# Kernel tuning notes

Hardware: AMD Instinct MI355X
Metric: run time of the kernel (lower is better)

## Reference

```python
import jax, jax.numpy as jnp
import numpy as np

N_NODES = 100000
N_EDGES = 1600000
NUM_RELS = 8
IN_FEAT = 128
OUT_FEAT = 128


def setup_inputs() -> dict:
    key = jax.random.key(0)
    k1, k2, k3, k4, k5 = jax.random.split(key, 5)
    feat = jax.random.normal(k1, (N_NODES, IN_FEAT), dtype=jnp.float32)
    weight = jax.random.normal(k2, (NUM_RELS, IN_FEAT, OUT_FEAT), dtype=jnp.float32) * 0.05
    src = jax.random.randint(k3, (N_EDGES,), 0, N_NODES, dtype=jnp.int64 if jax.config.jax_enable_x64 else jnp.int32)
    dst = jax.random.randint(k4, (N_EDGES,), 0, N_NODES, dtype=jnp.int64 if jax.config.jax_enable_x64 else jnp.int32)
    etypes = jax.random.randint(k5, (N_EDGES,), 0, NUM_RELS, dtype=jnp.int64 if jax.config.jax_enable_x64 else jnp.int32)
    return {"feat": feat, "weight": weight, "src": src, "dst": dst, "etypes": etypes}


def reference(feat, weight, src, dst, etypes):
    # RGCN segment_mm: per edge e, message m_e = feat[src[e]] @ weight[etypes[e]],
    # then sum-aggregate messages into destination nodes.
    # The torch module sorts edges by etype only so segment_mm can run a grouped
    # GEMM; the scatter-sum aggregation is order-independent, so sorting does not
    # change the math. We compute all per-relation projections densely (small R)
    # and gather the right one per edge -- equivalent math, fully vectorized.
    proj = jnp.einsum('ni,rio->rno', feat, weight)      # [R, N, out]
    m = proj[etypes, src]                               # [E, out] gather per edge
    out = jax.ops.segment_sum(m, dst, num_segments=feat.shape[0])  # [N, out]
    return out
```

## Files before the change

kernel.cpp:

```cpp
#include <hip/hip_runtime.h>
#include <hip/hip_bf16.h>


#define FEAT 128
#define LDG 136
#define LDSS 136
#define CAP 512
#define CHUNK 128

typedef __attribute__((ext_vector_type(8))) short short8;
typedef __attribute__((ext_vector_type(8))) __bf16 bf16x8;
typedef __attribute__((ext_vector_type(4))) float f32x4;

__device__ __forceinline__ unsigned f2bf(float x) {
    union { float f; unsigned u; } v; v.f = x;
    unsigned r = v.u + 0x7FFFu + ((v.u >> 16) & 1u);
    return r >> 16;
}

__global__ void cvt_feat_kernel(const float* __restrict__ f,
                                ushort* __restrict__ o, int n8) {
    int i = blockIdx.x * blockDim.x + threadIdx.x;
    if (i >= n8) return;
    const float4* f4 = (const float4*)f;
    float4 a = f4[2 * i], b = f4[2 * i + 1];
    union { ushort u[8]; int4 v; } pk;
    pk.u[0] = f2bf(a.x); pk.u[1] = f2bf(a.y); pk.u[2] = f2bf(a.z); pk.u[3] = f2bf(a.w);
    pk.u[4] = f2bf(b.x); pk.u[5] = f2bf(b.y); pk.u[6] = f2bf(b.z); pk.u[7] = f2bf(b.w);
    ((int4*)o)[i] = pk.v;
}

__global__ void cvt_w_kernel(const float* __restrict__ w,
                             ushort* __restrict__ wt, int total, int KW) {
    int i = blockIdx.x * blockDim.x + threadIdx.x;
    if (i >= total) return;
    int n = i / KW;
    int rk = i - n * KW;
    int r = rk >> 7, k = rk & 127;
    wt[i] = (ushort)f2bf(w[(r << 14) + (k << 7) + n]);
}

__global__ void scatter_kernel(const int* __restrict__ dst,
                               const int* __restrict__ et,
                               const int* __restrict__ src, int E, int R,
                               int sbits, int* __restrict__ cursor,
                               int* __restrict__ recs) {
    int i = blockIdx.x * blockDim.x + threadIdx.x;
    int stride = gridDim.x * blockDim.x;
    for (; i < E; i += stride) {
        int d = dst[i];
        int b = (d >> 7) * R + et[i];
        int p = atomicAdd(&cursor[b], 1);
        if (p < CAP) recs[(size_t)b * CAP + p] = src[i] | ((d & 127) << sbits);
    }
}

__global__ __launch_bounds__(256, 2)
void fused_kernel(const ushort* __restrict__ featb,
                  const ushort* __restrict__ wtb,
                  const int* __restrict__ recs,
                  const int* __restrict__ cursor,
                  float* __restrict__ out, int N, int R, int KW, int sbits) {
    __shared__ __align__(16) ushort GS[CHUNK * LDG];
    __shared__ __align__(16) ushort dlv[CHUNK];

    int t = threadIdx.x;
    int qid = t >> 4, c = t & 15;
    int lane = t & 63, wid = t >> 6;
    int lm = lane & 15, lq = lane >> 4;
    int blk = blockIdx.x, base = blk * 128;
    int mq = (wid >> 1) * 64, nq = (wid & 1) * 64;
    int smask = (1 << sbits) - 1;

    f32x4 acc[16];
    #pragma unroll
    for (int i = 0; i < 16; i++) acc[i] = (f32x4){0.f, 0.f, 0.f, 0.f};

    for (int r = 0; r < R; r++) {
        int bkt = blk * R + r;
        int ecnt = cursor[bkt];
        if (ecnt <= 0) continue;
        if (ecnt > CAP) ecnt = CAP;
        const int* rb = recs + (size_t)bkt * CAP;

        f32x4 accS[16];
        #pragma unroll
        for (int i = 0; i < 16; i++) accS[i] = (f32x4){0.f, 0.f, 0.f, 0.f};

        for (int c0 = 0; c0 < ecnt; c0 += CHUNK) {
            int rcv[8]; uint4 gvv[8];
            #pragma unroll
            for (int p = 0; p < 8; p++) {
                int j = c0 + p * 16 + qid;
                rcv[p] = (j < ecnt) ? rb[j] : -1;
            }
            #pragma unroll
            for (int p = 0; p < 8; p++) {
                if (rcv[p] >= 0)
                    gvv[p] = *(const uint4*)(featb +
                             (size_t)(rcv[p] & smask) * FEAT + c * 8);
                else
                    gvv[p] = (uint4){0u, 0u, 0u, 0u};
            }
            #pragma unroll
            for (int p = 0; p < 8; p++)
                *(uint4*)&GS[(p * 16 + qid) * LDG + c * 8] = gvv[p];
            if (c == 0) {
                #pragma unroll
                for (int p = 0; p < 8; p++)
                    dlv[p * 16 + qid] = (rcv[p] >= 0)
                        ? (ushort)((rcv[p] >> sbits) & 127) : (ushort)0xFFFF;
            }
            __syncthreads();

            #pragma unroll
            for (int ks = 0; ks < 4; ks++) {
                int kof = ks * 32 + lq * 8;
                union { ushort u[8]; uint4 v; } dlw;
                dlw.v = *(const uint4*)&dlv[kof];
                short8 paf[4];
                #pragma unroll
                for (int tm = 0; tm < 4; tm++) {
                    ushort row = (ushort)(mq + tm * 16 + lm);
                    union { ushort u[8]; short8 s; } pa;
                    #pragma unroll
                    for (int q = 0; q < 8; q++)
                        pa.u[q] = (dlw.u[q] == row) ? (ushort)0x3F80 : (ushort)0;
                    paf[tm] = pa.s;
                }
                short8 bgf[4];
                #pragma unroll
                for (int tn = 0; tn < 4; tn++) {
                    int col = nq + tn * 16 + lm;
                    union { ushort u[8]; short8 s; } bb;
                    #pragma unroll
                    for (int q = 0; q < 8; q++)
                        bb.u[q] = GS[(kof + q) * LDG + col];
                    bgf[tn] = bb.s;
                }
                #pragma unroll
                for (int tm = 0; tm < 4; tm++)
                    #pragma unroll
                    for (int tn = 0; tn < 4; tn++)
                        accS[tm * 4 + tn] = __builtin_amdgcn_mfma_f32_16x16x32_bf16(
                            __builtin_bit_cast(bf16x8, paf[tm]),
                            __builtin_bit_cast(bf16x8, bgf[tn]),
                            accS[tm * 4 + tn], 0, 0, 0);
            }
            __syncthreads();
        }

        #pragma unroll
        for (int tm = 0; tm < 4; tm++)
            #pragma unroll
            for (int tn = 0; tn < 4; tn++)
                #pragma unroll
                for (int i = 0; i < 4; i++) {
                    int row = mq + tm * 16 + lq * 4 + i;
                    int col = nq + tn * 16 + lm;
                    GS[row * LDSS + col] = (ushort)f2bf(accS[tm * 4 + tn][i]);
                }
        __syncthreads();

        const ushort* bp = wtb + (size_t)(nq + lm) * KW + r * FEAT;
        #pragma unroll
        for (int ks = 0; ks < 4; ks++) {
            int kof = ks * 32 + lq * 8;
            short8 af[4], bfg[4];
            #pragma unroll
            for (int tm = 0; tm < 4; tm++)
                af[tm] = *(const short8*)&GS[(mq + tm * 16 + lm) * LDSS + kof];
            #pragma unroll
            for (int tn = 0; tn < 4; tn++)
                bfg[tn] = *(const short8*)(bp + (size_t)(tn * 16) * KW + kof);
            #pragma unroll
            for (int tm = 0; tm < 4; tm++)
                #pragma unroll
                for (int tn = 0; tn < 4; tn++)
                    acc[tm * 4 + tn] = __builtin_amdgcn_mfma_f32_16x16x32_bf16(
                        __builtin_bit_cast(bf16x8, af[tm]),
                        __builtin_bit_cast(bf16x8, bfg[tn]),
                        acc[tm * 4 + tn], 0, 0, 0);
        }
        __syncthreads();
    }

    #pragma unroll
    for (int tm = 0; tm < 4; tm++) {
        #pragma unroll
        for (int i = 0; i < 4; i++) {
            int row = base + mq + tm * 16 + lq * 4 + i;
            if (row < N) {
                float* op = out + (size_t)row * FEAT + nq + lm;
                #pragma unroll
                for (int tn = 0; tn < 4; tn++) op[tn * 16] = acc[tm * 4 + tn][i];
            }
        }
    }
}

static inline size_t al256(size_t x) { return (x + 255) & ~(size_t)255; }

extern "C" void kernel_launch(void* const* d_in, const int* in_sizes, int n_in,
                              void* d_out, int out_size, void* d_ws,
                              size_t ws_size, hipStream_t stream) {
    const float* feat = (const float*)d_in[0];
    const float* weight = (const float*)d_in[1];
    const int* src = (const int*)d_in[2];
    const int* dst = (const int*)d_in[3];
    const int* et = (const int*)d_in[4];

    int nfeat = in_sizes[0];
    int N = nfeat / FEAT;
    int R = in_sizes[1] / (FEAT * FEAT);
    int E = in_sizes[2];
    int Npad = ((N + 127) / 128) * 128;
    int nblk = Npad / 128;
    int NB = nblk * R;
    int KW = R * FEAT;
    float* out = (float*)d_out;

    int sbits = 1;
    while ((1 << sbits) < N) sbits++;

    char* ws = (char*)d_ws;
    size_t o = 0;
    size_t cur_o  = o; o += al256((size_t)NB * 4);
    size_t recs_o = o; o += al256((size_t)NB * CAP * 4);
    size_t wtb_o  = o; o += al256((size_t)R * FEAT * FEAT * 2);
    size_t featb_o = o;

    int* cursor = (int*)(ws + cur_o);
    int* recs   = (int*)(ws + recs_o);
    ushort* wtb   = (ushort*)(ws + wtb_o);
    ushort* featb = (ushort*)(ws + featb_o);

    hipMemsetAsync(cursor, 0, (size_t)NB * 4, stream);

    int wtotal = R * FEAT * FEAT;
    cvt_w_kernel<<<(wtotal + 255) / 256, 256, 0, stream>>>(weight, wtb, wtotal, KW);
    int n8 = nfeat / 8;
    cvt_feat_kernel<<<(n8 + 255) / 256, 256, 0, stream>>>(feat, featb, n8);

    scatter_kernel<<<512, 256, 0, stream>>>(dst, et, src, E, R, sbits,
                                            cursor, recs);

    fused_kernel<<<nblk, 256, 0, stream>>>(featb, wtb, recs, cursor,
                                           out, N, R, KW, sbits);
}
```

Baseline: 425.9 us.

## Reorder to transform-then-scatter per chunk with register prefetch of next gather

Each 128-edge chunk is now first multiplied by the relation weight (gathered features times W) into a transposed LDS tile, then scattered into destination rows through a one-hot MFMA. Before, the one-hot aggregation ran first and the weight GEMM ran once per relation. The next chunk's record indices and feature rows are prefetched into registers while the current chunk computes, hiding gather latency. Output stores become vectorized f32x4 writes. The cost is a second LDS buffer, more registers, and a weight GEMM per chunk instead of per relation, which adds MFMA work whenever a bucket holds more than one chunk.

```diff
diff --git a/kernel.cpp b/kernel.cpp
--- a/kernel.cpp
+++ b/kernel.cpp
@@ -4,13 +4,14 @@
 
 #define FEAT 128
 #define LDG 136
-#define LDSS 136
+#define LDT 136
 #define CAP 512
 #define CHUNK 128
 
 typedef __attribute__((ext_vector_type(8))) short short8;
 typedef __attribute__((ext_vector_type(8))) __bf16 bf16x8;
 typedef __attribute__((ext_vector_type(4))) float f32x4;
+typedef __attribute__((ext_vector_type(2))) unsigned int uint2v;
 
 __device__ __forceinline__ unsigned f2bf(float x) {
     union { float f; unsigned u; } v; v.f = x;
@@ -61,7 +62,8 @@
                   const int* __restrict__ recs,
                   const int* __restrict__ cursor,
                   float* __restrict__ out, int N, int R, int KW, int sbits) {
-    __shared__ __align__(16) ushort GS[CHUNK * LDG];
+    __shared__ __align__(16) ushort G[CHUNK * LDG];
+    __shared__ __align__(16) ushort Tt[FEAT * LDT];
     __shared__ __align__(16) ushort dlv[CHUNK];
 
     int t = threadIdx.x;
@@ -69,7 +71,10 @@
     int lane = t & 63, wid = t >> 6;
     int lm = lane & 15, lq = lane >> 4;
     int blk = blockIdx.x, base = blk * 128;
-    int mq = (wid >> 1) * 64, nq = (wid & 1) * 64;
+    int er = (wid >> 1) * 64;
+    int nw = (wid & 1) * 64;
+    int fr = (wid >> 1) * 64;
+    int dc = (wid & 1) * 64;
     int smask = (1 << sbits) - 1;
 
     f32x4 acc[16];
@@ -83,28 +88,31 @@
         if (ecnt > CAP) ecnt = CAP;
         const int* rb = recs + (size_t)bkt * CAP;
 
-        f32x4 accS[16];
+        int rcv[8]; uint4 gvv[8];
         #pragma unroll
-        for (int i = 0; i < 16; i++) accS[i] = (f32x4){0.f, 0.f, 0.f, 0.f};
+        for (int p = 0; p < 8; p++) {
+            int j = p * 16 + qid;
+            rcv[p] = (j < ecnt) ? rb[j] : -1;
+        }
+        #pragma unroll
+        for (int p = 0; p < 8; p++) {
+            if (rcv[p] >= 0)
+                gvv[p] = *(const uint4*)(featb +
+                         (size_t)(rcv[p] & smask) * FEAT + c * 8);
+            else
+                gvv[p] = (uint4){0u, 0u, 0u, 0u};
+        }
 
         for (int c0 = 0; c0 < ecnt; c0 += CHUNK) {
-            int rcv[8]; uint4 gvv[8];
+            int rcvn[8];
             #pragma unroll
             for (int p = 0; p < 8; p++) {
-                int j = c0 + p * 16 + qid;
-                rcv[p] = (j < ecnt) ? rb[j] : -1;
-            }
-            #pragma unroll
-            for (int p = 0; p < 8; p++) {
-                if (rcv[p] >= 0)
-                    gvv[p] = *(const uint4*)(featb +
-                             (size_t)(rcv[p] & smask) * FEAT + c * 8);
-                else
-                    gvv[p] = (uint4){0u, 0u, 0u, 0u};
+                int j = c0 + CHUNK + p * 16 + qid;
+                rcvn[p] = (j < ecnt) ? rb[j] : -1;
             }
             #pragma unroll
             for (int p = 0; p < 8; p++)
-                *(uint4*)&GS[(p * 16 + qid) * LDG + c * 8] = gvv[p];
+                *(uint4*)&G[(p * 16 + qid) * LDG + c * 8] = gvv[p];
             if (c == 0) {
                 #pragma unroll
                 for (int p = 0; p < 8; p++)
@@ -113,87 +121,96 @@
             }
             __syncthreads();
 
+            uint4 gvvn[8];
+            #pragma unroll
+            for (int p = 0; p < 8; p++) {
+                if (rcvn[p] >= 0)
+                    gvvn[p] = *(const uint4*)(featb +
+                              (size_t)(rcvn[p] & smask) * FEAT + c * 8);
+                else
+                    gvvn[p] = (uint4){0u, 0u, 0u, 0u};
+            }
+
+            f32x4 Ta[16];
+            #pragma unroll
+            for (int i = 0; i < 16; i++) Ta[i] = (f32x4){0.f, 0.f, 0.f, 0.f};
+            const ushort* bpw = wtb + (size_t)(nw + lm) * KW + r * FEAT;
             #pragma unroll
             for (int ks = 0; ks < 4; ks++) {
                 int kof = ks * 32 + lq * 8;
-                union { ushort u[8]; uint4 v; } dlw;
-                dlw.v = *(const uint4*)&dlv[kof];
-                short8 paf[4];
-                #pragma unroll
-                for (int tm = 0; tm < 4; tm++) {
-                    ushort row = (ushort)(mq + tm * 16 + lm);
-                    union { ushort u[8]; short8 s; } pa;
+                short8 af[4], bw[4];
+                #pragma unroll
+                for (int tm = 0; tm < 4; tm++)
+                    af[tm] = *(const short8*)&G[(er + tm * 16 + lm) * LDG + kof];
+                #pragma unroll
+                for (int tn = 0; tn < 4; tn++)
+                    bw[tn] = *(const short8*)(bpw + (size_t)(tn * 16) * KW + kof);
+                #pragma unroll
+                for (int tm = 0; tm < 4; tm++)
+                    #pragma unroll
+                    for (int tn = 0; tn < 4; tn++)
+                        Ta[tm * 4 + tn] = __builtin_amdgcn_mfma_f32_16x16x32_bf16(
+                            __builtin_bit_cast(bf16x8, af[tm]),
+                            __builtin_bit_cast(bf16x8, bw[tn]),
+                            Ta[tm * 4 + tn], 0, 0, 0);
+            }
+
+            #pragma unroll
+            for (int tm = 0; tm < 4; tm++)
+                #pragma unroll
+                for (int tn = 0; tn < 4; tn++) {
+                    f32x4 v = Ta[tm * 4 + tn];
+                    union { unsigned u[2]; uint2v w; } pk;
+                    pk.u[0] = f2bf(v[0]) | (f2bf(v[1]) << 16);
+                    pk.u[1] = f2bf(v[2]) | (f2bf(v[3]) << 16);
+                    *(uint2v*)&Tt[(nw + tn * 16 + lm) * LDT +
+                                  er + tm * 16 + lq * 4] = pk.w;
+                }
+            __syncthreads();
+
+            #pragma unroll
+            for (int ks = 0; ks < 4; ks++) {
+                int kof = ks * 32 + lq * 8;
+                union { ushort u[8]; uint4 v; } dl8;
+                dl8.v = *(const uint4*)&dlv[kof];
+                short8 at[4];
+                #pragma unroll
+                for (int tm = 0; tm < 4; tm++)
+                    at[tm] = *(const short8*)&Tt[(fr + tm * 16 + lm) * LDT + kof];
+                short8 pb[4];
+                #pragma unroll
+                for (int tn = 0; tn < 4; tn++) {
+                    ushort col = (ushort)(dc + tn * 16 + lm);
+                    union { ushort u[8]; short8 s; } b;
                     #pragma unroll
                     for (int q = 0; q < 8; q++)
-                        pa.u[q] = (dlw.u[q] == row) ? (ushort)0x3F80 : (ushort)0;
-                    paf[tm] = pa.s;
-                }
-                short8 bgf[4];
-                #pragma unroll
-                for (int tn = 0; tn < 4; tn++) {
-                    int col = nq + tn * 16 + lm;
-                    union { ushort u[8]; short8 s; } bb;
-                    #pragma unroll
-                    for (int q = 0; q < 8; q++)
-                        bb.u[q] = GS[(kof + q) * LDG + col];
-                    bgf[tn] = bb.s;
+                        b.u[q] = (dl8.u[q] == col) ? (ushort)0x3F80 : (ushort)0;
+                    pb[tn] = b.s;
                 }
                 #pragma unroll
                 for (int tm = 0; tm < 4; tm++)
                     #pragma unroll
                     for (int tn = 0; tn < 4; tn++)
-                        accS[tm * 4 + tn] = __builtin_amdgcn_mfma_f32_16x16x32_bf16(
-                            __builtin_bit_cast(bf16x8, paf[tm]),
-                            __builtin_bit_cast(bf16x8, bgf[tn]),
-                            accS[tm * 4 + tn], 0, 0, 0);
+                        acc[tm * 4 + tn] = __builtin_amdgcn_mfma_f32_16x16x32_bf16(
+                            __builtin_bit_cast(bf16x8, at[tm]),
+                            __builtin_bit_cast(bf16x8, pb[tn]),
+                            acc[tm * 4 + tn], 0, 0, 0);
             }
             __syncthreads();
-        }
-
-        #pragma unroll
-        for (int tm = 0; tm < 4; tm++)
-            #pragma unroll
-            for (int tn = 0; tn < 4; tn++)
-                #pragma unroll
-                for (int i = 0; i < 4; i++) {
-                    int row = mq + tm * 16 + lq * 4 + i;
-                    int col = nq + tn * 16 + lm;
-                    GS[row * LDSS + col] = (ushort)f2bf(accS[tm * 4 + tn][i]);
-                }
-        __syncthreads();
-
-        const ushort* bp = wtb + (size_t)(nq + lm) * KW + r * FEAT;
-        #pragma unroll
-        for (int ks = 0; ks < 4; ks++) {
-            int kof = ks * 32 + lq * 8;
-            short8 af[4], bfg[4];
-            #pragma unroll
-            for (int tm = 0; tm < 4; tm++)
-                af[tm] = *(const short8*)&GS[(mq + tm * 16 + lm) * LDSS + kof];
-            #pragma unroll
-            for (int tn = 0; tn < 4; tn++)
-                bfg[tn] = *(const short8*)(bp + (size_t)(tn * 16) * KW + kof);
-            #pragma unroll
-            for (int tm = 0; tm < 4; tm++)
-                #pragma unroll
-                for (int tn = 0; tn < 4; tn++)
-                    acc[tm * 4 + tn] = __builtin_amdgcn_mfma_f32_16x16x32_bf16(
-                        __builtin_bit_cast(bf16x8, af[tm]),
-                        __builtin_bit_cast(bf16x8, bfg[tn]),
-                        acc[tm * 4 + tn], 0, 0, 0);
-        }
-        __syncthreads();
+
+            #pragma unroll
+            for (int p = 0; p < 8; p++) { rcv[p] = rcvn[p]; gvv[p] = gvvn[p]; }
+        }
     }
 
     #pragma unroll
-    for (int tm = 0; tm < 4; tm++) {
-        #pragma unroll
-        for (int i = 0; i < 4; i++) {
-            int row = base + mq + tm * 16 + lq * 4 + i;
-            if (row < N) {
-                float* op = out + (size_t)row * FEAT + nq + lm;
-                #pragma unroll
-                for (int tn = 0; tn < 4; tn++) op[tn * 16] = acc[tm * 4 + tn][i];
+    for (int tn = 0; tn < 4; tn++) {
+        int drow = base + dc + tn * 16 + lm;
+        if (drow < N) {
+            #pragma unroll
+            for (int tm = 0; tm < 4; tm++) {
+                f32x4 v = acc[tm * 4 + tn];
+                *(f32x4*)(out + (size_t)drow * FEAT + fr + tm * 16 + lq * 4) = v;
             }
         }
     }
```

Result: slower. 787.3 us (+84.8%).
